# Performance work log

Measured on AMD Instinct MI355X. Metric: run time of the kernel, lower is better.

Reference implementation:

```python
import jax, jax.numpy as jnp
import numpy as np

T, B, F_IN = 1024, 256, 87


def _lstm(x, Wih, Whh, b):
    """PyTorch-convention LSTM over seq-first x [T,B,In]; gate order i,f,g,o."""
    H = Whh.shape[1]
    Bz = x.shape[1]

    def step(carry, xt):
        h, c = carry
        z = xt @ Wih.T + h @ Whh.T + b  # [B, 4H]
        i, f, g, o = jnp.split(z, 4, axis=-1)
        c = jax.nn.sigmoid(f) * c + jax.nn.sigmoid(i) * jnp.tanh(g)
        h = jax.nn.sigmoid(o) * jnp.tanh(c)
        return (h, c), h

    init = (jnp.zeros((Bz, H), x.dtype), jnp.zeros((Bz, H), x.dtype))
    _, ys = jax.lax.scan(step, init, x)
    return ys  # [T, B, H]


def setup_inputs() -> dict:
    key = jax.random.key(0)
    ks = jax.random.split(key, 24)

    def p(k, shape, fan):
        s = 1.0 / np.sqrt(fan)
        return jax.random.uniform(k, shape, jnp.float32, -s, s)

    d = {}
    d["x"] = jax.random.normal(ks[0], (T, B, F_IN), jnp.float32)
    # LSTM params (bias = b_ih + b_hh combined; forward-equivalent)
    dims = [(F_IN, 256), (256, 128), (128, 64), (64, 32)]
    ki = 1
    for li, (din, h) in enumerate(dims, start=1):
        d[f"w{li}i"] = p(ks[ki], (4 * h, din), h); ki += 1
        d[f"w{li}h"] = p(ks[ki], (4 * h, h), h); ki += 1
        d[f"b{li}"] = p(ks[ki], (4 * h,), h); ki += 1
    fcs = [(32, 128), (128, 64), (64, 32), (32, 3)]
    for fi, (din, dout) in enumerate(fcs, start=1):
        d[f"f{fi}w"] = p(ks[ki], (dout, din), din); ki += 1
        d[f"f{fi}b"] = p(ks[ki], (dout,), din); ki += 1
    return d


def reference(x, w1i, w1h, b1, w2i, w2h, b2, w3i, w3h, b3, w4i, w4h, b4,
              f1w, f1b, f2w, f2b, f3w, f3b, f4w, f4b):
    h = jnp.tanh(_lstm(x, w1i, w1h, b1))
    h = jnp.tanh(_lstm(h, w2i, w2h, b2))
    h = jnp.tanh(_lstm(h, w3i, w3h, b3))
    h = jnp.tanh(_lstm(h, w4i, w4h, b4)[0])  # [0] -> first timestep, [B,32]
    h = jax.nn.relu(h @ f1w.T + f1b)
    h = jax.nn.relu(h @ f2w.T + f2b)
    h = jax.nn.relu(h @ f3w.T + f3b)
    return h @ f4w.T + f4b  # [B, 3]
```

## Files before the change

kernel.cpp:

```cpp
#include <hip/hip_runtime.h>
#include <math.h>


#define O_W1T 0
#define O_W2T 66816
#define O_W3T 165120
#define O_W4T 189696
#define O_F1T 195840
#define O_F2T 199936
#define O_F3T 208128
#define O_B1  210176
#define O_B2  210944
#define O_B3  211328
#define O_B4  211520

__global__ __launch_bounds__(256) void prep_kernel(
    const float* __restrict__ w1i, const float* __restrict__ w2i,
    const float* __restrict__ w3i, const float* __restrict__ w4i,
    const float* __restrict__ b1,  const float* __restrict__ b2,
    const float* __restrict__ b3,  const float* __restrict__ b4,
    const float* __restrict__ f1w, const float* __restrict__ f2w,
    const float* __restrict__ f3w, float* __restrict__ ws)
{
    int i = blockIdx.x * 256 + threadIdx.x;
    if (i < 89088) {
        int row = i / 87, k = i - row * 87;
        int g = row >> 8;
        if (g != 1) {
            int base = (g == 0) ? 0 : (g == 2) ? 256 : 512;
            ws[O_W1T + k * 768 + base + (row & 255)] = w1i[i];
        }
    } else if (i < 220160) {
        int l = i - 89088;
        int row = l >> 8, k = l & 255;
        int g = row >> 7;
        if (g != 1) {
            int base = (g == 0) ? 0 : (g == 2) ? 128 : 256;
            ws[O_W2T + k * 384 + base + (row & 127)] = w2i[l];
        }
    } else if (i < 252928) {
        int l = i - 220160;
        int row = l >> 7, k = l & 127;
        int g = row >> 6;
        if (g != 1) {
            int base = (g == 0) ? 0 : (g == 2) ? 64 : 128;
            ws[O_W3T + k * 192 + base + (row & 63)] = w3i[l];
        }
    } else if (i < 261120) {
        int l = i - 252928;
        int row = l >> 6, k = l & 63;
        int g = row >> 5;
        if (g != 1) {
            int base = (g == 0) ? 0 : (g == 2) ? 32 : 64;
            ws[O_W4T + k * 96 + base + (row & 31)] = w4i[l];
        }
    } else if (i < 262144) {
        int l = i - 261120;
        int g = l >> 8;
        if (g != 1) {
            int base = (g == 0) ? 0 : (g == 2) ? 256 : 512;
            ws[O_B1 + base + (l & 255)] = b1[l];
        }
    } else if (i < 262656) {
        int l = i - 262144;
        int g = l >> 7;
        if (g != 1) {
            int base = (g == 0) ? 0 : (g == 2) ? 128 : 256;
            ws[O_B2 + base + (l & 127)] = b2[l];
        }
    } else if (i < 262912) {
        int l = i - 262656;
        int g = l >> 6;
        if (g != 1) {
            int base = (g == 0) ? 0 : (g == 2) ? 64 : 128;
            ws[O_B3 + base + (l & 63)] = b3[l];
        }
    } else if (i < 263040) {
        int l = i - 262912;
        int g = l >> 5;
        if (g != 1) {
            int base = (g == 0) ? 0 : (g == 2) ? 32 : 64;
            ws[O_B4 + base + (l & 31)] = b4[l];
        }
    } else if (i < 267136) {
        int l = i - 263040;
        int j = l >> 5, k = l & 31;
        ws[O_F1T + k * 128 + j] = f1w[l];
    } else if (i < 275328) {
        int l = i - 267136;
        int j = l >> 7, k = l & 127;
        ws[O_F2T + k * 64 + j] = f2w[l];
    } else if (i < 277376) {
        int l = i - 275328;
        int j = l >> 6, k = l & 63;
        ws[O_F3T + k * 32 + j] = f3w[l];
    }
}

__device__ __forceinline__ float frcp(float x) { return __builtin_amdgcn_rcpf(x); }
__device__ __forceinline__ float sigm(float x) { return frcp(1.0f + __expf(-x)); }
__device__ __forceinline__ float tanh_f(float x) { return 1.0f - 2.0f * frcp(1.0f + __expf(2.0f * x)); }
__device__ __forceinline__ float cell(float zi, float zg, float zo) {
    float c = sigm(zi) * tanh_f(zg);
    return tanh_f(sigm(zo) * tanh_f(c));
}

__global__ __launch_bounds__(512) void lstm_fused(
    const float* __restrict__ x, const float* __restrict__ ws,
    const float* __restrict__ f1b, const float* __restrict__ f2b,
    const float* __restrict__ f3b, const float* __restrict__ f4w,
    const float* __restrict__ f4b, float* __restrict__ out)
{
    const int t = threadIdx.x;
    const int r = blockIdx.x;

    __shared__ float xs[87];
    __shared__ float h1[256], h2[128], h3[64], h4[32];
    __shared__ float a1[128], a2[64], a3[32];
    __shared__ float ps[1536];

    const float* W1T = ws + O_W1T;
    const float* W2T = ws + O_W2T;
    const float* W3T = ws + O_W3T;
    const float* W4T = ws + O_W4T;
    const float* F1T = ws + O_F1T;
    const float* F2T = ws + O_F2T;
    const float* F3T = ws + O_F3T;
    const float* B1p = ws + O_B1;
    const float* B2p = ws + O_B2;
    const float* B3p = ws + O_B3;
    const float* B4p = ws + O_B4;

    if (t < 87) xs[t] = x[r * 87 + t];
    __syncthreads();

    {
        const int j = t & 255, q = t >> 8;
        float zi = q ? 0.0f : B1p[j];
        float zg = q ? 0.0f : B1p[256 + j];
        float zo = q ? 0.0f : B1p[512 + j];
        const float* w = W1T + j;
        const int k0 = q ? 44 : 0, k1 = q ? 87 : 44;
        #pragma unroll 8
        for (int k = k0; k < k1; ++k) {
            const float xv = xs[k];
            zi = fmaf(xv, w[k * 768],       zi);
            zg = fmaf(xv, w[k * 768 + 256], zg);
            zo = fmaf(xv, w[k * 768 + 512], zo);
        }
        ps[q * 768 + j]       = zi;
        ps[q * 768 + 256 + j] = zg;
        ps[q * 768 + 512 + j] = zo;
    }
    __syncthreads();
    if (t < 256)
        h1[t] = cell(ps[t] + ps[768 + t],
                     ps[256 + t] + ps[1024 + t],
                     ps[512 + t] + ps[1280 + t]);
    __syncthreads();

    {
        const int j = t & 127, q = t >> 7;
        float zi = q ? 0.0f : B2p[j];
        float zg = q ? 0.0f : B2p[128 + j];
        float zo = q ? 0.0f : B2p[256 + j];
        const float* w = W2T + j;
        const int k0 = q * 64;
        #pragma unroll 8
        for (int k = k0; k < k0 + 64; ++k) {
            const float hv = h1[k];
            zi = fmaf(hv, w[k * 384],       zi);
            zg = fmaf(hv, w[k * 384 + 128], zg);
            zo = fmaf(hv, w[k * 384 + 256], zo);
        }
        ps[q * 384 + j]       = zi;
        ps[q * 384 + 128 + j] = zg;
        ps[q * 384 + 256 + j] = zo;
    }
    __syncthreads();
    if (t < 128) {
        float zi = 0.0f, zg = 0.0f, zo = 0.0f;
        #pragma unroll
        for (int q = 0; q < 4; ++q) {
            zi += ps[q * 384 + t];
            zg += ps[q * 384 + 128 + t];
            zo += ps[q * 384 + 256 + t];
        }
        h2[t] = cell(zi, zg, zo);
    }
    __syncthreads();

    {
        const int j = t & 63, q = t >> 6;
        float zi = q ? 0.0f : B3p[j];
        float zg = q ? 0.0f : B3p[64 + j];
        float zo = q ? 0.0f : B3p[128 + j];
        const float* w = W3T + j;
        const int k0 = q * 16;
        #pragma unroll
        for (int k = k0; k < k0 + 16; ++k) {
            const float hv = h2[k];
            zi = fmaf(hv, w[k * 192],       zi);
            zg = fmaf(hv, w[k * 192 + 64],  zg);
            zo = fmaf(hv, w[k * 192 + 128], zo);
        }
        ps[q * 192 + j]       = zi;
        ps[q * 192 + 64 + j]  = zg;
        ps[q * 192 + 128 + j] = zo;
    }
    __syncthreads();
    if (t < 64) {
        float zi = 0.0f, zg = 0.0f, zo = 0.0f;
        #pragma unroll
        for (int q = 0; q < 8; ++q) {
            zi += ps[q * 192 + t];
            zg += ps[q * 192 + 64 + t];
            zo += ps[q * 192 + 128 + t];
        }
        h3[t] = cell(zi, zg, zo);
    }
    __syncthreads();

    {
        const int j = t & 31, q = t >> 5;
        float zi = (q == 0) ? B4p[j] : 0.0f;
        float zg = (q == 0) ? B4p[32 + j] : 0.0f;
        float zo = (q == 0) ? B4p[64 + j] : 0.0f;
        const float* w = W4T + j;
        const int k0 = q * 4;
        #pragma unroll
        for (int k = k0; k < k0 + 4; ++k) {
            const float hv = h3[k];
            zi = fmaf(hv, w[k * 96],      zi);
            zg = fmaf(hv, w[k * 96 + 32], zg);
            zo = fmaf(hv, w[k * 96 + 64], zo);
        }
        ps[q * 96 + j]      = zi;
        ps[q * 96 + 32 + j] = zg;
        ps[q * 96 + 64 + j] = zo;
    }
    __syncthreads();
    if (t < 32) {
        float zi = 0.0f, zg = 0.0f, zo = 0.0f;
        #pragma unroll
        for (int q = 0; q < 16; ++q) {
            zi += ps[q * 96 + t];
            zg += ps[q * 96 + 32 + t];
            zo += ps[q * 96 + 64 + t];
        }
        h4[t] = cell(zi, zg, zo);
    }
    __syncthreads();

    {
        const int j = t & 127, q = t >> 7;
        float a = q ? 0.0f : f1b[j];
        const int k0 = q * 8;
        #pragma unroll
        for (int k = k0; k < k0 + 8; ++k)
            a = fmaf(h4[k], F1T[k * 128 + j], a);
        ps[q * 128 + j] = a;
    }
    __syncthreads();
    if (t < 128)
        a1[t] = fmaxf(ps[t] + ps[128 + t] + ps[256 + t] + ps[384 + t], 0.0f);
    __syncthreads();

    {
        const int j = t & 63, q = t >> 6;
        float a = q ? 0.0f : f2b[j];
        const int k0 = q * 16;
        #pragma unroll
        for (int k = k0; k < k0 + 16; ++k)
            a = fmaf(a1[k], F2T[k * 64 + j], a);
        ps[q * 64 + j] = a;
    }
    __syncthreads();
    if (t < 64) {
        float a = 0.0f;
        #pragma unroll
        for (int q = 0; q < 8; ++q) a += ps[q * 64 + t];
        a2[t] = fmaxf(a, 0.0f);
    }
    __syncthreads();

    {
        const int j = t & 31, q = t >> 5;
        float a = (q == 0) ? f3b[j] : 0.0f;
        const int k0 = q * 4;
        #pragma unroll
        for (int k = k0; k < k0 + 4; ++k)
            a = fmaf(a2[k], F3T[k * 32 + j], a);
        ps[q * 32 + j] = a;
    }
    __syncthreads();
    if (t < 32) {
        float a = 0.0f;
        #pragma unroll
        for (int q = 0; q < 16; ++q) a += ps[q * 32 + t];
        a3[t] = fmaxf(a, 0.0f);
    }
    __syncthreads();

    if (t < 3) {
        float a = f4b[t];
        const float* w = f4w + t * 32;
        #pragma unroll
        for (int k = 0; k < 32; ++k)
            a = fmaf(a3[k], w[k], a);
        out[r * 3 + t] = a;
    }
}

extern "C" void kernel_launch(void* const* d_in, const int* in_sizes, int n_in,
                              void* d_out, int out_size, void* d_ws, size_t ws_size,
                              hipStream_t stream) {
    const float* x   = (const float*)d_in[0];
    const float* w1i = (const float*)d_in[1];
    const float* b1  = (const float*)d_in[3];
    const float* w2i = (const float*)d_in[4];
    const float* b2  = (const float*)d_in[6];
    const float* w3i = (const float*)d_in[7];
    const float* b3  = (const float*)d_in[9];
    const float* w4i = (const float*)d_in[10];
    const float* b4  = (const float*)d_in[12];
    const float* f1w = (const float*)d_in[13];
    const float* f1b = (const float*)d_in[14];
    const float* f2w = (const float*)d_in[15];
    const float* f2b = (const float*)d_in[16];
    const float* f3w = (const float*)d_in[17];
    const float* f3b = (const float*)d_in[18];
    const float* f4w = (const float*)d_in[19];
    const float* f4b = (const float*)d_in[20];
    float* ws  = (float*)d_ws;
    float* out = (float*)d_out;

    prep_kernel<<<1084, 256, 0, stream>>>(w1i, w2i, w3i, w4i, b1, b2, b3, b4,
                                          f1w, f2w, f3w, ws);
    lstm_fused<<<256, 512, 0, stream>>>(x, ws, f1b, f2b, f3b, f4w, f4b, out);
}
```

Measured before the change: 166.5 us.

## Split LSTM layers across 4-block groups with global-flag sync and float4 weights

Each group of four blocks now handles four batch rows together. Each block computes a quarter of the layer-1 and layer-2 gate columns, so each weight load is reused across four rows. Partial hidden states go to global workspace, and the blocks synchronise through atomic flags and spin-waits. Weight reads use float4 vectors. The inter-block spin-wait depends on all four blocks of a group being resident at once, which holds with 256 blocks on this GPU, and it adds atomic and flag-reset overhead.

```diff
diff --git a/kernel.cpp b/kernel.cpp
--- a/kernel.cpp
+++ b/kernel.cpp
@@ -13,6 +13,9 @@
 #define O_B2  210944
 #define O_B3  211328
 #define O_B4  211520
+#define O_FLG 211616
+#define O_H1  211744
+#define O_H2  277280
 
 __global__ __launch_bounds__(256) void prep_kernel(
     const float* __restrict__ w1i, const float* __restrict__ w2i,
@@ -23,6 +26,7 @@
     const float* __restrict__ f3w, float* __restrict__ ws)
 {
     int i = blockIdx.x * 256 + threadIdx.x;
+    if (i < 128) ((int*)ws)[O_FLG + i] = 0;
     if (i < 89088) {
         int row = i / 87, k = i - row * 87;
         int g = row >> 8;
@@ -105,19 +109,25 @@
     return tanh_f(sigm(zo) * tanh_f(c));
 }
 
-__global__ __launch_bounds__(512) void lstm_fused(
-    const float* __restrict__ x, const float* __restrict__ ws,
+#define FMA4(z, xv, wv) \
+    z.x = fmaf(xv, wv.x, z.x); z.y = fmaf(xv, wv.y, z.y); \
+    z.z = fmaf(xv, wv.z, z.z); z.w = fmaf(xv, wv.w, z.w);
+
+__global__ __launch_bounds__(512) void lstm_fused_sliced(
+    const float* __restrict__ x, float* __restrict__ ws,
     const float* __restrict__ f1b, const float* __restrict__ f2b,
     const float* __restrict__ f3b, const float* __restrict__ f4w,
     const float* __restrict__ f4b, float* __restrict__ out)
 {
     const int t = threadIdx.x;
-    const int r = blockIdx.x;
-
-    __shared__ float xs[87];
-    __shared__ float h1[256], h2[128], h3[64], h4[32];
-    __shared__ float a1[128], a2[64], a3[32];
-    __shared__ float ps[1536];
+    const int g = blockIdx.x >> 2;
+    const int s = blockIdx.x & 3;
+    const int row = blockIdx.x;
+
+    __shared__ __align__(16) float xs4[348];
+    __shared__ __align__(16) float buf[1536];
+    __shared__ __align__(16) float hbuf[1024];
+    __shared__ float h3s[64], h4s[32], a1s[128], a2s[64], a3s[32];
 
     const float* W1T = ws + O_W1T;
     const float* W2T = ws + O_W2T;
@@ -126,189 +136,252 @@
     const float* F1T = ws + O_F1T;
     const float* F2T = ws + O_F2T;
     const float* F3T = ws + O_F3T;
-    const float* B1p = ws + O_B1;
-    const float* B2p = ws + O_B2;
-    const float* B3p = ws + O_B3;
-    const float* B4p = ws + O_B4;
-
-    if (t < 87) xs[t] = x[r * 87 + t];
-    __syncthreads();
-
+    int* flg1 = (int*)ws + O_FLG + g;
+    int* flg2 = (int*)ws + O_FLG + 64 + g;
+
+    if (t < 348) xs4[t] = x[g * 348 + t];
+
+    float b1i = 0.f, b1g = 0.f, b1o = 0.f;
+    float b2i = 0.f, b2g = 0.f, b2o = 0.f;
+    float b3i = 0.f, b3g = 0.f, b3o = 0.f;
+    float b4i = 0.f, b4g = 0.f, b4o = 0.f;
+    float vf1 = 0.f, vf2 = 0.f, vf3 = 0.f;
     {
-        const int j = t & 255, q = t >> 8;
-        float zi = q ? 0.0f : B1p[j];
-        float zg = q ? 0.0f : B1p[256 + j];
-        float zo = q ? 0.0f : B1p[512 + j];
-        const float* w = W1T + j;
-        const int k0 = q ? 44 : 0, k1 = q ? 87 : 44;
-        #pragma unroll 8
+        const float* B1p = ws + O_B1;
+        const float* B2p = ws + O_B2;
+        const float* B3p = ws + O_B3;
+        const float* B4p = ws + O_B4;
+        int j6 = t & 63, j5 = t & 31;
+        if (t < 256) { b1i = B1p[s*64+j6]; b1g = B1p[256+s*64+j6]; b1o = B1p[512+s*64+j6]; }
+        if (t < 128) { b2i = B2p[s*32+j5]; b2g = B2p[128+s*32+j5]; b2o = B2p[256+s*32+j5]; vf1 = f1b[t]; }
+        if (t < 64)  { b3i = B3p[t]; b3g = B3p[64+t]; b3o = B3p[128+t]; vf2 = f2b[t]; }
+        if (t < 32)  { b4i = B4p[t]; b4g = B4p[32+t]; b4o = B4p[64+t]; vf3 = f3b[t]; }
+    }
+    __syncthreads();
+
+    if (t < 384) {
+        const int kk = t / 192;
+        const int u  = t - kk * 192;
+        const int r  = u / 48;
+        const int v  = u - r * 48;
+        const int gate = v >> 4, q = v & 15;
+        const int col = gate * 256 + s * 64 + q * 4;
+        const float* wp = W1T + col;
+        const float* xr = xs4 + r * 87;
+        const int k0 = kk ? 44 : 0, k1 = kk ? 87 : 44;
+        float4 z = {0.f, 0.f, 0.f, 0.f};
+        #pragma unroll 4
         for (int k = k0; k < k1; ++k) {
-            const float xv = xs[k];
-            zi = fmaf(xv, w[k * 768],       zi);
-            zg = fmaf(xv, w[k * 768 + 256], zg);
-            zo = fmaf(xv, w[k * 768 + 512], zo);
-        }
-        ps[q * 768 + j]       = zi;
-        ps[q * 768 + 256 + j] = zg;
-        ps[q * 768 + 512 + j] = zo;
-    }
-    __syncthreads();
-    if (t < 256)
-        h1[t] = cell(ps[t] + ps[768 + t],
-                     ps[256 + t] + ps[1024 + t],
-                     ps[512 + t] + ps[1280 + t]);
-    __syncthreads();
-
-    {
-        const int j = t & 127, q = t >> 7;
-        float zi = q ? 0.0f : B2p[j];
-        float zg = q ? 0.0f : B2p[128 + j];
-        float zo = q ? 0.0f : B2p[256 + j];
-        const float* w = W2T + j;
-        const int k0 = q * 64;
-        #pragma unroll 8
+            const float4 wv = *(const float4*)(wp + k * 768);
+            const float xv = xr[k];
+            FMA4(z, xv, wv);
+        }
+        *(float4*)&buf[kk * 768 + r * 192 + gate * 64 + q * 4] = z;
+    }
+    __syncthreads();
+    if (t < 256) {
+        const int r = t >> 6, j = t & 63;
+        const float zi = buf[r*192 + j]       + buf[768 + r*192 + j]       + b1i;
+        const float zg = buf[r*192 + 64 + j]  + buf[768 + r*192 + 64 + j]  + b1g;
+        const float zo = buf[r*192 + 128 + j] + buf[768 + r*192 + 128 + j] + b1o;
+        const float h = cell(zi, zg, zo);
+        __hip_atomic_store(&ws[O_H1 + (4*g + r) * 256 + s * 64 + j], h,
+                           __ATOMIC_RELAXED, __HIP_MEMORY_SCOPE_AGENT);
+    }
+    __syncthreads();
+    if (t == 0)
+        __hip_atomic_fetch_add(flg1, 1, __ATOMIC_RELEASE, __HIP_MEMORY_SCOPE_AGENT);
+
+    if (t == 0) {
+        while (__hip_atomic_load(flg1, __ATOMIC_RELAXED, __HIP_MEMORY_SCOPE_AGENT) < 4)
+            __builtin_amdgcn_s_sleep(2);
+        (void)__hip_atomic_load(flg1, __ATOMIC_ACQUIRE, __HIP_MEMORY_SCOPE_AGENT);
+    }
+    __syncthreads();
+    for (int i = t; i < 1024; i += 512)
+        hbuf[i] = __hip_atomic_load(&ws[O_H1 + g * 1024 + i],
+                                    __ATOMIC_RELAXED, __HIP_MEMORY_SCOPE_AGENT);
+    __syncthreads();
+
+    if (t < 384) {
+        const int kk = t / 96;
+        const int u  = t - kk * 96;
+        const int r  = u / 24;
+        const int v  = u - r * 24;
+        const int gate = v >> 3, q = v & 7;
+        const int col = gate * 128 + s * 32 + q * 4;
+        const float* wp = W2T + col;
+        const float* hr = hbuf + r * 256;
+        const int k0 = kk * 64;
+        float4 z = {0.f, 0.f, 0.f, 0.f};
+        #pragma unroll 4
         for (int k = k0; k < k0 + 64; ++k) {
-            const float hv = h1[k];
-            zi = fmaf(hv, w[k * 384],       zi);
-            zg = fmaf(hv, w[k * 384 + 128], zg);
-            zo = fmaf(hv, w[k * 384 + 256], zo);
-        }
-        ps[q * 384 + j]       = zi;
-        ps[q * 384 + 128 + j] = zg;
-        ps[q * 384 + 256 + j] = zo;
+            const float4 wv = *(const float4*)(wp + k * 384);
+            const float hv = hr[k];
+            FMA4(z, hv, wv);
+        }
+        *(float4*)&buf[kk * 384 + r * 96 + gate * 32 + q * 4] = z;
     }
     __syncthreads();
     if (t < 128) {
-        float zi = 0.0f, zg = 0.0f, zo = 0.0f;
-        #pragma unroll
-        for (int q = 0; q < 4; ++q) {
-            zi += ps[q * 384 + t];
-            zg += ps[q * 384 + 128 + t];
-            zo += ps[q * 384 + 256 + t];
-        }
-        h2[t] = cell(zi, zg, zo);
-    }
-    __syncthreads();
-
-    {
-        const int j = t & 63, q = t >> 6;
-        float zi = q ? 0.0f : B3p[j];
-        float zg = q ? 0.0f : B3p[64 + j];
-        float zo = q ? 0.0f : B3p[128 + j];
-        const float* w = W3T + j;
-        const int k0 = q * 16;
+        const int r = t >> 5, j = t & 31;
+        float zi = b2i, zg = b2g, zo = b2o;
+        #pragma unroll
+        for (int kk = 0; kk < 4; ++kk) {
+            zi += buf[kk*384 + r*96 + j];
+            zg += buf[kk*384 + r*96 + 32 + j];
+            zo += buf[kk*384 + r*96 + 64 + j];
+        }
+        const float h = cell(zi, zg, zo);
+        __hip_atomic_store(&ws[O_H2 + (4*g + r) * 128 + s * 32 + j], h,
+                           __ATOMIC_RELAXED, __HIP_MEMORY_SCOPE_AGENT);
+    }
+    __syncthreads();
+    if (t == 0)
+        __hip_atomic_fetch_add(flg2, 1, __ATOMIC_RELEASE, __HIP_MEMORY_SCOPE_AGENT);
+
+    if (t == 0) {
+        while (__hip_atomic_load(flg2, __ATOMIC_RELAXED, __HIP_MEMORY_SCOPE_AGENT) < 4)
+            __builtin_amdgcn_s_sleep(2);
+        (void)__hip_atomic_load(flg2, __ATOMIC_ACQUIRE, __HIP_MEMORY_SCOPE_AGENT);
+    }
+    __syncthreads();
+    if (t < 128)
+        hbuf[t] = __hip_atomic_load(&ws[O_H2 + row * 128 + t],
+                                    __ATOMIC_RELAXED, __HIP_MEMORY_SCOPE_AGENT);
+    __syncthreads();
+
+    if (t < 384) {
+        const int kk = t / 48, Q = t - kk * 48;
+        const float* wp = W3T + 4 * Q;
+        const int k0 = kk * 16;
+        float4 z = {0.f, 0.f, 0.f, 0.f};
         #pragma unroll
         for (int k = k0; k < k0 + 16; ++k) {
-            const float hv = h2[k];
-            zi = fmaf(hv, w[k * 192],       zi);
-            zg = fmaf(hv, w[k * 192 + 64],  zg);
-            zo = fmaf(hv, w[k * 192 + 128], zo);
-        }
-        ps[q * 192 + j]       = zi;
-        ps[q * 192 + 64 + j]  = zg;
-        ps[q * 192 + 128 + j] = zo;
+            const float4 wv = *(const float4*)(wp + k * 192);
+            const float hv = hbuf[k];
+            FMA4(z, hv, wv);
+        }
+        *(float4*)&buf[kk * 192 + 4 * Q] = z;
     }
     __syncthreads();
     if (t < 64) {
-        float zi = 0.0f, zg = 0.0f, zo = 0.0f;
-        #pragma unroll
-        for (int q = 0; q < 8; ++q) {
-            zi += ps[q * 192 + t];
-            zg += ps[q * 192 + 64 + t];
-            zo += ps[q * 192 + 128 + t];
-        }
-        h3[t] = cell(zi, zg, zo);
-    }
-    __syncthreads();
-
-    {
-        const int j = t & 31, q = t >> 5;
-        float zi = (q == 0) ? B4p[j] : 0.0f;
-        float zg = (q == 0) ? B4p[32 + j] : 0.0f;
-        float zo = (q == 0) ? B4p[64 + j] : 0.0f;
-        const float* w = W4T + j;
-        const int k0 = q * 4;
+        float zi = b3i, zg = b3g, zo = b3o;
+        #pragma unroll
+        for (int kk = 0; kk < 8; ++kk) {
+            zi += buf[kk*192 + t];
+            zg += buf[kk*192 + 64 + t];
+            zo += buf[kk*192 + 128 + t];
+        }
+        h3s[t] = cell(zi, zg, zo);
+    }
+    __syncthreads();
+
+    if (t < 384) {
+        const int kk = t / 24, Q = t - kk * 24;
+        const float* wp = W4T + 4 * Q;
+        const int k0 = kk * 4;
+        float4 z = {0.f, 0.f, 0.f, 0.f};
         #pragma unroll
         for (int k = k0; k < k0 + 4; ++k) {
-            const float hv = h3[k];
-            zi = fmaf(hv, w[k * 96],      zi);
-            zg = fmaf(hv, w[k * 96 + 32], zg);
-            zo = fmaf(hv, w[k * 96 + 64], zo);
-        }
-        ps[q * 96 + j]      = zi;
-        ps[q * 96 + 32 + j] = zg;
-        ps[q * 96 + 64 + j] = zo;
+            const float4 wv = *(const float4*)(wp + k * 96);
+            const float hv = h3s[k];
+            FMA4(z, hv, wv);
+        }
+        *(float4*)&buf[kk * 96 + 4 * Q] = z;
     }
     __syncthreads();
     if (t < 32) {
-        float zi = 0.0f, zg = 0.0f, zo = 0.0f;
-        #pragma unroll
-        for (int q = 0; q < 16; ++q) {
-            zi += ps[q * 96 + t];
-            zg += ps[q * 96 + 32 + t];
-            zo += ps[q * 96 + 64 + t];
-        }
-        h4[t] = cell(zi, zg, zo);
-    }
-    __syncthreads();
-
-    {
-        const int j = t & 127, q = t >> 7;
-        float a = q ? 0.0f : f1b[j];
-        const int k0 = q * 8;
-        #pragma unroll
-        for (int k = k0; k < k0 + 8; ++k)
-            a = fmaf(h4[k], F1T[k * 128 + j], a);
-        ps[q * 128 + j] = a;
-    }
-    __syncthreads();
-    if (t < 128)
-        a1[t] = fmaxf(ps[t] + ps[128 + t] + ps[256 + t] + ps[384 + t], 0.0f);
-    __syncthreads();
-
-    {
-        const int j = t & 63, q = t >> 6;
-        float a = q ? 0.0f : f2b[j];
-        const int k0 = q * 16;
-        #pragma unroll
-        for (int k = k0; k < k0 + 16; ++k)
-            a = fmaf(a1[k], F2T[k * 64 + j], a);
-        ps[q * 64 + j] = a;
+        float zi = b4i, zg = b4g, zo = b4o;
+        #pragma unroll
+        for (int kk = 0; kk < 16; ++kk) {
+            zi += buf[kk*96 + t];
+            zg += buf[kk*96 + 32 + t];
+            zo += buf[kk*96 + 64 + t];
+        }
+        h4s[t] = cell(zi, zg, zo);
+    }
+    __syncthreads();
+
+    if (t < 256) {
+        const int kk = t >> 5, Q = t & 31;
+        const float* wp = F1T + 4 * Q;
+        const int k0 = kk * 4;
+        float4 z = {0.f, 0.f, 0.f, 0.f};
+        #pragma unroll
+        for (int k = k0; k < k0 + 4; ++k) {
+            const float4 wv = *(const float4*)(wp + k * 128);
+            const float hv = h4s[k];
+            FMA4(z, hv, wv);
+        }
+        *(float4*)&buf[kk * 128 + 4 * Q] = z;
+    }
+    __syncthreads();
+    if (t < 128) {
+        float a = vf1;
+        #pragma unroll
+        for (int kk = 0; kk < 8; ++kk) a += buf[kk*128 + t];
+        a1s[t] = fmaxf(a, 0.0f);
+    }
+    __syncthreads();
+
+    if (t < 256) {
+        const int kk = t >> 4, Q = t & 15;
+        const float* wp = F2T + 4 * Q;
+        const int k0 = kk * 8;
+        float4 z = {0.f, 0.f, 0.f, 0.f};
+        #pragma unroll
+        for (int k = k0; k < k0 + 8; ++k) {
+            const float4 wv = *(const float4*)(wp + k * 64);
+            const float hv = a1s[k];
+            FMA4(z, hv, wv);
+        }
+        *(float4*)&buf[kk * 64 + 4 * Q] = z;
     }
     __syncthreads();
     if (t < 64) {
-        float a = 0.0f;
-        #pragma unroll
-        for (int q = 0; q < 8; ++q) a += ps[q * 64 + t];
-        a2[t] = fmaxf(a, 0.0f);
-    }
-    __syncthreads();
-
-    {
-        const int j = t & 31, q = t >> 5;
-        float a = (q == 0) ? f3b[j] : 0.0f;
-        const int k0 = q * 4;
-        #pragma unroll
-        for (int k = k0; k < k0 + 4; ++k)
-            a = fmaf(a2[k], F3T[k * 32 + j], a);
-        ps[q * 32 + j] = a;
+        float a = vf2;
+        #pragma unroll
+        for (int kk = 0; kk < 16; ++kk) a += buf[kk*64 + t];
+        a2s[t] = fmaxf(a, 0.0f);
+    }
+    __syncthreads();
+
+    if (t < 128) {
+        const int kk = t >> 3, Q = t & 7;
+        const float* wp = F3T + 4 * Q;
+        const int k0 = kk * 4;
+        float4 z = {0.f, 0.f, 0.f, 0.f};
+        #pragma unroll
+        for (int k = k0; k < k0 + 4; ++k) {
+            const float4 wv = *(const float4*)(wp + k * 32);
+            const float hv = a2s[k];
+            FMA4(z, hv, wv);
+        }
+        *(float4*)&buf[kk * 32 + 4 * Q] = z;
     }
     __syncthreads();
     if (t < 32) {
-        float a = 0.0f;
-        #pragma unroll
-        for (int q = 0; q < 16; ++q) a += ps[q * 32 + t];
-        a3[t] = fmaxf(a, 0.0f);
+        float a = vf3;
+        #pragma unroll
+        for (int kk = 0; kk < 16; ++kk) a += buf[kk*32 + t];
+        a3s[t] = fmaxf(a, 0.0f);
     }
     __syncthreads();
 
     if (t < 3) {
-        float a = f4b[t];
-        const float* w = f4w + t * 32;
-        #pragma unroll
-        for (int k = 0; k < 32; ++k)
-            a = fmaf(a3[k], w[k], a);
-        out[r * 3 + t] = a;
+        const float4* wr = (const float4*)(f4w + t * 32);
+        float a0 = f4b[t], a1 = 0.f;
+        #pragma unroll
+        for (int i = 0; i < 8; ++i) {
+            const float4 wv = wr[i];
+            const float4 hv = *(const float4*)&a3s[4 * i];
+            a0 = fmaf(hv.x, wv.x, a0);
+            a1 = fmaf(hv.y, wv.y, a1);
+            a0 = fmaf(hv.z, wv.z, a0);
+            a1 = fmaf(hv.w, wv.w, a1);
+        }
+        out[row * 3 + t] = a0 + a1;
     }
 }
 
@@ -337,5 +410,6 @@
 
     prep_kernel<<<1084, 256, 0, stream>>>(w1i, w2i, w3i, w4i, b1, b2, b3, b4,
                                           f1w, f2w, f3w, ws);
-    lstm_fused<<<256, 512, 0, stream>>>(x, ws, f1b, f2b, f3b, f4w, f4b, out);
+    lstm_fused_sliced<<<256, 512, 0, stream>>>(x, ws, f1b, f2b, f3b, f4w, f4b,
+                                               out);
 }
```

After: 178.9 us. +7.5%, slower.
